# Performance work log

Hardware: AMD Instinct MI355X
Metric: run time of the kernel (lower is better)

The kernel has to match this reference:

```python
import jax, jax.numpy as jnp
import numpy as np

NUM_CLASSES = 2
TOP_K = 1500
CONF_THRESH = 0.01
NMS_THRESH = 0.2
VAR0, VAR1 = 0.1, 0.2  # cfg['variance']


def setup_inputs() -> dict:
    key = jax.random.key(0)
    k1, k2, k3 = jax.random.split(key, 3)
    B, P = 32, 76800
    loc_data = jax.random.normal(k1, (B, P, 4), jnp.float32)
    conf_data = jax.random.uniform(k2, (B * P, NUM_CLASSES), jnp.float32)
    prior_data = jax.random.uniform(k3, (P, 4), jnp.float32)
    return {"loc_data": loc_data, "conf_data": conf_data, "prior_data": prior_data}


def _decode(loc, priors):
    # loc, priors: [P,4]; SSD box decode with variances
    cxcy = priors[:, :2] + loc[:, :2] * VAR0 * priors[:, 2:]
    wh = priors[:, 2:] * jnp.exp(loc[:, 2:] * VAR1)
    x1y1 = cxcy - wh * 0.5
    return jnp.concatenate([x1y1, x1y1 + wh], axis=-1)  # [P,4] (x1,y1,x2,y2)


def _nms_per_class(scores, boxes):
    # scores: [P], boxes: [P,4] -> [TOP_K,5] packed (score,x1,y1,x2,y2)
    s = jnp.where(scores > CONF_THRESH, scores, -jnp.inf)
    sk, idx = jax.lax.top_k(s, TOP_K)  # torch nms keeps only top_k candidates
    bk = boxes[idx]
    x1, y1, x2, y2 = bk[:, 0], bk[:, 1], bk[:, 2], bk[:, 3]
    area = (x2 - x1) * (y2 - y1)
    iota = jnp.arange(TOP_K)

    def step(active, i):
        # greedy NMS over score-descending candidates
        xx1 = jnp.maximum(x1, x1[i]); yy1 = jnp.maximum(y1, y1[i])
        xx2 = jnp.minimum(x2, x2[i]); yy2 = jnp.minimum(y2, y2[i])
        inter = jnp.maximum(xx2 - xx1, 0.0) * jnp.maximum(yy2 - yy1, 0.0)
        iou = inter / (area + area[i] - inter)
        kept = active[i]
        suppress = (iou > NMS_THRESH) & (iota != i)
        active = jnp.where(kept, active & ~suppress, active)
        return active, kept

    _, keep = jax.lax.scan(step, sk > -jnp.inf, iota)
    rows = jnp.where(keep[:, None], jnp.concatenate([sk[:, None], bk], axis=1), 0.0)
    # pack kept rows at the front (score-descending order), zeros after
    rank = jnp.cumsum(keep) - 1
    dest = jnp.where(keep, rank, TOP_K)  # dump non-kept into scratch slot
    return jnp.zeros((TOP_K + 1, 5), bk.dtype).at[dest].set(rows)[:TOP_K]


def reference(loc_data, conf_data, prior_data):
    B, P, _ = loc_data.shape
    conf = conf_data.reshape(B, P, NUM_CLASSES)
    decoded = jax.vmap(_decode, in_axes=(0, None))(loc_data, prior_data)  # [B,P,4]
    outs = []
    for cl in range(1, NUM_CLASSES):  # background class 0 stays zero
        outs.append(jax.vmap(_nms_per_class)(conf[:, :, cl], decoded))
    bg = jnp.zeros((B, 1, TOP_K, 5), decoded.dtype)
    return jnp.concatenate([bg, jnp.stack(outs, axis=1)], axis=1)  # [B,C,TOP_K,5]
```

## Files before the change

### kernel.cpp

```cpp
#include <hip/hip_runtime.h>
#include <stdint.h>

typedef unsigned long long u64;
typedef unsigned int u32;

#define NUM_B 32
#define NUM_P 76800
#define TOPK 1500
#define NBINS 2048
#define CAP 2048
#define NWORDS 24
#define NCHUNK 6
#define HSLICES 16
#define HCHUNK (NUM_P / HSLICES)
#define NPAIR 276

__device__ __forceinline__ u32 fbits(float f) { return __float_as_uint(f); }
__device__ __forceinline__ int binOf(float s) {
    int b = (int)(s * (float)NBINS);
    return (b > NBINS - 1) ? NBINS - 1 : b;
}
__device__ __forceinline__ u64 readlane64(u64 v, int l) {
    u32 lo = (u32)__builtin_amdgcn_readlane((int)(u32)(v & 0xffffffffu), l);
    u32 hi = (u32)__builtin_amdgcn_readlane((int)(u32)(v >> 32), l);
    return ((u64)hi << 32) | lo;
}

__global__ __launch_bounds__(256) void hist_kernel(const float4* __restrict__ conf4,
                                                   u32* __restrict__ hist,
                                                   u32* __restrict__ bpos) {
    int c = blockIdx.x, b = blockIdx.y, tid = threadIdx.x;
    if (tid < NBINS / HSLICES) bpos[(size_t)b * NBINS + c * (NBINS / HSLICES) + tid] = 0;
    __shared__ u32 h[NBINS];
    for (int i = tid; i < NBINS; i += 256) h[i] = 0;
    __syncthreads();
    const float4* base = conf4 + (size_t)b * (NUM_P / 2) + (size_t)c * (HCHUNK / 2);
    for (int i = tid; i < HCHUNK / 2; i += 256) {
        float4 v = base[i];
        if (v.y > 0.01f) atomicAdd(&h[binOf(v.y)], 1u);
        if (v.w > 0.01f) atomicAdd(&h[binOf(v.w)], 1u);
    }
    __syncthreads();
    u32* outp = hist + ((size_t)b * HSLICES + c) * NBINS;
    for (int i = tid; i < NBINS; i += 256) outp[i] = h[i];
}

__global__ void thresh_kernel(const u32* __restrict__ hist, int* __restrict__ tbin,
                              u32* __restrict__ binbase, u32* __restrict__ bincnt,
                              u32* __restrict__ ntotal) {
    int b = blockIdx.x;
    int tid = threadIdx.x;
    const u32* hb = hist + (size_t)b * HSLICES * NBINS;
    __shared__ u32 vals[256];
    __shared__ int s_min;
    u32 total = 0;
    for (int c = 0; c < NBINS / 256; ++c) {
        if (tid == 0) s_min = 256;
        int bin = NBINS - 1 - (c * 256 + tid);
        u32 v = 0;
#pragma unroll
        for (int s = 0; s < HSLICES; ++s) v += hb[(size_t)s * NBINS + bin];
        __syncthreads();
        vals[tid] = v;
        __syncthreads();
        for (int off = 1; off < 256; off <<= 1) {
            u32 add = (tid >= off) ? vals[tid - off] : 0;
            __syncthreads();
            vals[tid] += add;
            __syncthreads();
        }
        u32 cum = total + vals[tid];
        binbase[(size_t)b * NBINS + bin] = cum - v;
        bincnt [(size_t)b * NBINS + bin] = v;
        if (cum >= TOPK) atomicMin(&s_min, tid);
        __syncthreads();
        if (s_min < 256) {
            if (tid == s_min) { tbin[b] = bin; ntotal[b] = cum; }
            return;
        }
        total += vals[255];
    }
    if (tid == 0) { tbin[b] = 0; ntotal[b] = total; }
}

__global__ __launch_bounds__(256) void compact_kernel(
    const float4* __restrict__ conf4, const int* __restrict__ tbin,
    const u32* __restrict__ binbase, u32* __restrict__ bpos,
    u64* __restrict__ keys) {
    int b = blockIdx.y;
    int tid = threadIdx.x;
    int f4 = blockIdx.x * 256 + tid;
    float4 c = conf4[(size_t)b * (NUM_P / 2) + f4];
    int tb = tbin[b];
    int p0 = f4 * 2, p1 = p0 + 1;

    int b0 = binOf(c.y);
    if (c.y > 0.01f && b0 >= tb) {
        u32 slot = atomicAdd(&bpos[(size_t)b * NBINS + b0], 1u);
        u32 pos = binbase[(size_t)b * NBINS + b0] + slot;
        if (pos < CAP) keys[(size_t)b * CAP + pos] = ((u64)fbits(c.y) << 32) | (u32)(~p0);
    }
    int b1 = binOf(c.w);
    if (c.w > 0.01f && b1 >= tb) {
        u32 slot = atomicAdd(&bpos[(size_t)b * NBINS + b1], 1u);
        u32 pos = binbase[(size_t)b * NBINS + b1] + slot;
        if (pos < CAP) keys[(size_t)b * CAP + pos] = ((u64)fbits(c.w) << 32) | (u32)(~p1);
    }
}

__global__ __launch_bounds__(256) void rank_decode_kernel(
    const u64* __restrict__ keys, const u32* __restrict__ binbase,
    const u32* __restrict__ bincnt, const u32* __restrict__ ntotal,
    const float* __restrict__ loc, const float* __restrict__ prior,
    float* __restrict__ sscore, float* __restrict__ sbox) {
#pragma clang fp contract(off)
    int b = blockIdx.y;
    int g = blockIdx.x * 256 + threadIdx.x;
    int n = (int)min(ntotal[b], (u32)CAP);
    if (g >= n) return;
    const u64* kb = keys + (size_t)b * CAP;
    u64 mykey = kb[g];
    float sc = __uint_as_float((u32)(mykey >> 32));
    int bn = binOf(sc);
    u32 start = binbase[(size_t)b * NBINS + bn];
    u32 end = start + bincnt[(size_t)b * NBINS + bn];
    if (end > (u32)n) end = (u32)n;
    u32 rank = start;
#pragma unroll 4
    for (u32 j = start; j < end; ++j) rank += (kb[j] > mykey) ? 1u : 0u;

    if (rank < TOPK) {
        u32 pidx = ~(u32)mykey;
        const float* lp = &loc[((size_t)b * NUM_P + pidx) * 4];
        const float* pp = &prior[(size_t)pidx * 4];
        float lx = lp[0], ly = lp[1], lw = lp[2], lh = lp[3];
        float pcx = pp[0], pcy = pp[1], pw = pp[2], ph = pp[3];
        float cx = pcx + (lx * 0.1f) * pw;
        float cy = pcy + (ly * 0.1f) * ph;
        float w  = pw * expf(lw * 0.2f);
        float h  = ph * expf(lh * 0.2f);
        float x1 = cx - w * 0.5f;
        float y1 = cy - h * 0.5f;
        float x2 = x1 + w;
        float y2 = y1 + h;
        sscore[(size_t)b * TOPK + rank] = sc;
        float* bx = &sbox[((size_t)b * TOPK + rank) * 4];
        bx[0] = x1; bx[1] = y1; bx[2] = x2; bx[3] = y2;
    }
}

__global__ __launch_bounds__(256) void mask_kernel(
    const float* __restrict__ sbox, u64* __restrict__ mask) {
#pragma clang fp contract(off)
    int w = blockIdx.x, c = blockIdx.y, b = blockIdx.z, tid = threadIdx.x;
    int i = c * 256 + tid;
    if ((w * 64 + 63) <= (c * 256)) return;
    __shared__ float4 cbox[64];
    __shared__ float car[64];
    if (tid < 64) {
        int j = w * 64 + tid;
        float4 bx = make_float4(0.f, 0.f, 0.f, 0.f);
        if (j < TOPK) bx = ((const float4*)sbox)[(size_t)b * TOPK + j];
        cbox[tid] = bx;
        car[tid] = (bx.z - bx.x) * (bx.w - bx.y);
    }
    __syncthreads();
    if (i < TOPK && (w * 64 + 63) > i) {
        const double MID = 0.5 * ((double)__uint_as_float(0x3E4CCCCDu) +
                                  (double)__uint_as_float(0x3E4CCCCEu));
        const float4 bx = ((const float4*)sbox)[(size_t)b * TOPK + i];
        float x1i = bx.x, y1i = bx.y, x2i = bx.z, y2i = bx.w;
        float ai = (x2i - x1i) * (y2i - y1i);
        u64 jmask = (i < w * 64) ? ~0ULL : (~0ULL << (i - w * 64 + 1));
        u64 m = 0;
        for (int j2 = 0; j2 < 64; ++j2) {
            float4 cb = cbox[j2];
            float xx1 = fmaxf(cb.x, x1i);
            float yy1 = fmaxf(cb.y, y1i);
            float xx2 = fminf(cb.z, x2i);
            float yy2 = fminf(cb.w, y2i);
            float iw = fmaxf(xx2 - xx1, 0.0f);
            float ih = fmaxf(yy2 - yy1, 0.0f);
            float inter = iw * ih;
            float denom = (car[j2] + ai) - inter;
            if ((double)inter >= MID * (double)denom) m |= (1ULL << j2);
        }
        m &= jmask;
        mask[((size_t)b * NWORDS + w) * TOPK + i] = m;
    }
}

__global__ __launch_bounds__(256) void sweep_kernel(
    const u64* __restrict__ mask, const float* __restrict__ sscore,
    const float* __restrict__ sbox, float* __restrict__ out) {
    int b = blockIdx.x, tid = threadIdx.x;
    int lane = tid & 63, wid = tid >> 6;

    const u64* mbase = mask + (size_t)b * NWORDS * TOPK;

    __shared__ u64 tb[NPAIR * 65];
    __shared__ u64 aw[NWORDS];
    __shared__ u32 pfx[NWORDS + 1];

    u64 act = 0;
    u64 dr[NWORDS];

    if (wid == 0) {
#pragma unroll
        for (int t = 0; t < NWORDS; ++t)
            dr[t] = mbase[(size_t)t * TOPK + t * 64 + lane];
        float sv[NWORDS];
#pragma unroll
        for (int c = 0; c < NWORDS; ++c) {
            int r = c * 64 + lane;
            sv[c] = (r < TOPK) ? sscore[(size_t)b * TOPK + r] : 0.0f;
        }
#pragma unroll
        for (int c = 0; c < NWORDS; ++c) {
            u64 m = __ballot(sv[c] > 0.0f);
            if (lane == c) act = m;
        }
    } else {
        int p0 = (wid - 1) * 92;
        int t = 0, rm = p0;
        while (rm >= NWORDS - 1 - t) { rm -= NWORDS - 1 - t; ++t; }
        int w = t + 1 + rm;
        int pbase = p0;
        for (int ch = 0; ch < 11; ++ch) {
            u64 tmp[8]; int lo[8];
#pragma unroll
            for (int k = 0; k < 8; ++k) {
                tmp[k] = mbase[(size_t)w * TOPK + t * 64 + lane];
                lo[k] = (pbase + k) * 65 + lane;
                if (++w == NWORDS) { ++t; w = t + 1; }
            }
#pragma unroll
            for (int k = 0; k < 8; ++k) tb[lo[k]] = tmp[k];
            pbase += 8;
        }
        {
            u64 tmp[4]; int lo[4];
#pragma unroll
            for (int k = 0; k < 4; ++k) {
                tmp[k] = mbase[(size_t)w * TOPK + t * 64 + lane];
                lo[k] = (pbase + k) * 65 + lane;
                if (++w == NWORDS) { ++t; w = t + 1; }
            }
#pragma unroll
            for (int k = 0; k < 4; ++k) tb[lo[k]] = tmp[k];
        }
    }
    __syncthreads();

    if (wid == 0) {
#pragma unroll
        for (int T = 0; T < NWORDS; ++T) {
            u64 dreg = dr[T];
            u64 actw = readlane64(act, T);
            u64 kept = 0, rem = actw;
            while (rem) {
                int i2 = __ffsll(rem) - 1;
                kept |= (1ULL << i2);
                rem &= rem - 1;
                rem &= ~readlane64(dreg, i2);
            }
            if (lane == T) act = kept;
            if (lane > T && lane < NWORDS) {
                const u64* rb = &tb[((T * (47 - T)) / 2 + (lane - T - 1)) * 65];
                u64 acc = 0;
#pragma unroll
                for (int b16 = 0; b16 < 4; ++b16) {
                    if ((u32)(kept >> (b16 * 16)) & 0xffffu) {
#pragma unroll
                        for (int j = 0; j < 16; ++j) {
                            int r = b16 * 16 + j;
                            u64 sel = (u64)0 - ((kept >> r) & 1ULL);
                            acc |= rb[r] & sel;
                        }
                    }
                }
                act &= ~acc;
            }
        }
        if (lane < NWORDS) aw[lane] = act;
    } else {
        float4* pz = (float4*)(out + (size_t)b * 2 * TOPK * 5);
        float4 z4 = make_float4(0.f, 0.f, 0.f, 0.f);
        for (int t2 = tid - 64; t2 < (2 * TOPK * 5) / 4; t2 += 192) pz[t2] = z4;
    }
    __syncthreads();
    if (tid == 0) {
        u32 acc = 0;
        for (int wd = 0; wd < NWORDS; ++wd) { pfx[wd] = acc; acc += (u32)__popcll(aw[wd]); }
        pfx[NWORDS] = acc;
    }
    __syncthreads();
    for (int r = tid; r < TOPK; r += 256) {
        int wd = r >> 6;
        u64 word = aw[wd];
        if ((word >> (r & 63)) & 1ULL) {
            u32 rank = pfx[wd] + (u32)__popcll(word & ((1ULL << (r & 63)) - 1ULL));
            float sc = sscore[(size_t)b * TOPK + r];
            float4 bx = ((const float4*)sbox)[(size_t)b * TOPK + r];
            size_t base_o = (((size_t)b * 2 + 1) * TOPK + (size_t)rank) * 5;
            out[base_o + 0] = sc;
            out[base_o + 1] = bx.x;
            out[base_o + 2] = bx.y;
            out[base_o + 3] = bx.z;
            out[base_o + 4] = bx.w;
        }
    }
}

extern "C" void kernel_launch(void* const* d_in, const int* in_sizes, int n_in,
                              void* d_out, int out_size, void* d_ws, size_t ws_size,
                              hipStream_t stream) {
    const float* loc   = (const float*)d_in[0];
    const float* conf  = (const float*)d_in[1];
    const float* prior = (const float*)d_in[2];
    float* out = (float*)d_out;
    char* ws = (char*)d_ws;

    u64* mask_buf = (u64*)(ws + 0);
    u32* hist     = (u32*)(ws + 0);
    u32* binbase  = (u32*)(ws + 4194304);
    u32* bincnt   = (u32*)(ws + 4456448);
    u32* bpos     = (u32*)(ws + 4718592);
    u64* keys     = (u64*)(ws + 4980736);
    int* tbin     = (int*)(ws + 5505024);
    u32* ntotal   = (u32*)(ws + 5505152);
    float* sscore = (float*)(ws + 9216000);
    float* sbox   = (float*)(ws + 9408000);

    hist_kernel<<<dim3(HSLICES, 32), 256, 0, stream>>>((const float4*)conf, hist, bpos);
    thresh_kernel<<<32, 256, 0, stream>>>(hist, tbin, binbase, bincnt, ntotal);
    compact_kernel<<<dim3(150, 32), 256, 0, stream>>>((const float4*)conf, tbin, binbase,
                                                      bpos, keys);
    rank_decode_kernel<<<dim3(CAP / 256, 32), 256, 0, stream>>>(keys, binbase, bincnt,
                                                                ntotal, loc, prior,
                                                                sscore, sbox);
    mask_kernel<<<dim3(NWORDS, NCHUNK, 32), 256, 0, stream>>>(sbox, mask_buf);
    sweep_kernel<<<32, 256, 0, stream>>>(mask_buf, sscore, sbox, out);
}
```

Measured before the change: 195.2 us.

## Parallelize NMS sweep diagonal resolution and cross-word suppression across wave lanes

Within the single-wave sequential NMS sweep, each diagonal 64-box block is now pre-resolved with wave-wide OR reductions. Boxes not suppressed by any active box are kept at once, and only the remaining unsafe candidates go through the serial ffs loop. The cross-word suppression OR over 64 rows, previously done by up to 23 lanes each scanning 64 rows, is split across lane groups and combined with shuffle trees. This shortens the serial critical path but adds shuffle and reduction overhead on each of the 24 steps. Lane 63 of the diagonal load is zeroed, apparently to avoid reading beyond valid data.

```diff
diff --git a/kernel.cpp b/kernel.cpp
--- a/kernel.cpp
+++ b/kernel.cpp
@@ -24,6 +24,21 @@
     u32 lo = (u32)__builtin_amdgcn_readlane((int)(u32)(v & 0xffffffffu), l);
     u32 hi = (u32)__builtin_amdgcn_readlane((int)(u32)(v >> 32), l);
     return ((u64)hi << 32) | lo;
+}
+__device__ __forceinline__ u64 shfl64(u64 v, int src) {
+    u32 lo = (u32)__shfl((int)(u32)(v & 0xffffffffu), src, 64);
+    u32 hi = (u32)__shfl((int)(u32)(v >> 32), src, 64);
+    return ((u64)hi << 32) | lo;
+}
+__device__ __forceinline__ u64 shflxor64(u64 v, int m) {
+    u32 lo = (u32)__shfl_xor((int)(u32)(v & 0xffffffffu), m, 64);
+    u32 hi = (u32)__shfl_xor((int)(u32)(v >> 32), m, 64);
+    return ((u64)hi << 32) | lo;
+}
+__device__ __forceinline__ u64 wave_or64(u64 v) {
+#pragma unroll
+    for (int s = 1; s < 64; s <<= 1) v |= shflxor64(v, s);
+    return v;
 }
 
 __global__ __launch_bounds__(256) void hist_kernel(const float4* __restrict__ conf4,
@@ -208,7 +223,7 @@
     if (wid == 0) {
 #pragma unroll
         for (int t = 0; t < NWORDS; ++t)
-            dr[t] = mbase[(size_t)t * TOPK + t * 64 + lane];
+            dr[t] = (lane < 63) ? mbase[(size_t)t * TOPK + t * 64 + lane] : 0ULL;
         float sv[NWORDS];
 #pragma unroll
         for (int c = 0; c < NWORDS; ++c) {
@@ -257,29 +272,47 @@
         for (int T = 0; T < NWORDS; ++T) {
             u64 dreg = dr[T];
             u64 actw = readlane64(act, T);
-            u64 kept = 0, rem = actw;
-            while (rem) {
-                int i2 = __ffsll(rem) - 1;
-                kept |= (1ULL << i2);
-                rem &= rem - 1;
-                rem &= ~readlane64(dreg, i2);
+            u64 mybit = (actw >> lane) & 1ULL;
+            u64 sup = wave_or64(mybit ? dreg : 0ULL);
+            u64 safe = actw & ~sup;
+            u64 unsafe = actw & sup;
+            u64 kept = safe;
+            if (unsafe) {
+                u64 msafe = wave_or64(((safe >> lane) & 1ULL) ? dreg : 0ULL);
+                u64 rem = unsafe & ~msafe;
+                while (rem) {
+                    int i2 = __ffsll(rem) - 1;
+                    kept |= (1ULL << i2);
+                    rem &= rem - 1;
+                    rem &= ~readlane64(dreg, i2);
+                }
             }
             if (lane == T) act = kept;
-            if (lane > T && lane < NWORDS) {
-                const u64* rb = &tb[((T * (47 - T)) / 2 + (lane - T - 1)) * 65];
+            const int nw = NWORDS - 1 - T;
+            if (nw > 0) {
+                const int G = (nw <= 1) ? 64 : (nw <= 2) ? 32 : (nw <= 4) ? 16
+                             : (nw <= 8) ? 8 : (nw <= 16) ? 4 : 2;
+                const int R = 64 / G;
+                int g = lane / nw;
+                int w = lane - g * nw;
                 u64 acc = 0;
-#pragma unroll
-                for (int b16 = 0; b16 < 4; ++b16) {
-                    if ((u32)(kept >> (b16 * 16)) & 0xffffu) {
-#pragma unroll
-                        for (int j = 0; j < 16; ++j) {
-                            int r = b16 * 16 + j;
-                            u64 sel = (u64)0 - ((kept >> r) & 1ULL);
-                            acc |= rb[r] & sel;
-                        }
+                if (g < G) {
+                    const u64* rbB = &tb[(size_t)(((T * (47 - T)) / 2 + w) * 65)];
+                    int r0 = g * R;
+#pragma unroll
+                    for (int jj = 0; jj < R; ++jj) {
+                        int r = r0 + jj;
+                        u64 sel = (u64)0 - ((kept >> r) & 1ULL);
+                        acc |= rbB[r] & sel;
                     }
                 }
-                act &= ~acc;
+#pragma unroll
+                for (int s = 1; s < G; s <<= 1)
+                    acc |= shfl64(acc, (g ^ s) * nw + w);
+                int srcl = lane - T - 1;
+                srcl = (srcl < 0 || srcl >= nw) ? 0 : srcl;
+                u64 supw = shfl64(acc, srcl);
+                if (lane > T && lane < NWORDS) act &= ~supw;
             }
         }
         if (lane < NWORDS) aw[lane] = act;
```

New measurement: 194.2 us. Within noise of the previous version (-0.6%).

## Widen sweep kernel to 1024 threads and add sparse-kept mask OR path

Applied to the files above, without the earlier changes.

The sweep kernel now launches 1024 threads per batch, so 15 loader waves each stage 19 mask tiles into shared memory instead of 3 waves staging 92, and the output zeroing moves into the load phase. Diagonal mask words are staged in shared memory rather than held in 24 registers, and the outer word loop is no longer unrolled, to relieve register pressure. The cross-word suppression uses a bit-iteration path when few boxes are kept, which avoids the full 64-row OR. Only 32 blocks are launched, so the serial wave-0 sweep remains the critical path, and the extra shared-memory reads may add latency.

```diff
diff --git a/kernel.cpp b/kernel.cpp
--- a/kernel.cpp
+++ b/kernel.cpp
@@ -190,7 +190,7 @@
     }
 }
 
-__global__ __launch_bounds__(256) void sweep_kernel(
+__global__ __launch_bounds__(1024) void sweep_kernel(
     const u64* __restrict__ mask, const float* __restrict__ sscore,
     const float* __restrict__ sbox, float* __restrict__ out) {
     int b = blockIdx.x, tid = threadIdx.x;
@@ -199,16 +199,18 @@
     const u64* mbase = mask + (size_t)b * NWORDS * TOPK;
 
     __shared__ u64 tb[NPAIR * 65];
+    __shared__ u64 td[NWORDS * 65];
     __shared__ u64 aw[NWORDS];
     __shared__ u32 pfx[NWORDS + 1];
 
     u64 act = 0;
-    u64 dr[NWORDS];
 
     if (wid == 0) {
 #pragma unroll
-        for (int t = 0; t < NWORDS; ++t)
-            dr[t] = mbase[(size_t)t * TOPK + t * 64 + lane];
+        for (int t = 0; t < NWORDS; ++t) {
+            u64 v = (lane < 63) ? mbase[(size_t)t * TOPK + t * 64 + lane] : 0ULL;
+            td[t * 65 + lane] = v;
+        }
         float sv[NWORDS];
 #pragma unroll
         for (int c = 0; c < NWORDS; ++c) {
@@ -221,41 +223,35 @@
             if (lane == c) act = m;
         }
     } else {
-        int p0 = (wid - 1) * 92;
+        int cnt = (wid == 15) ? (NPAIR - 14 * 19) : 19;
+        int p0 = (wid - 1) * 19;
         int t = 0, rm = p0;
         while (rm >= NWORDS - 1 - t) { rm -= NWORDS - 1 - t; ++t; }
         int w = t + 1 + rm;
-        int pbase = p0;
-        for (int ch = 0; ch < 11; ++ch) {
+        for (int base = 0; base < cnt; base += 8) {
+            int m = cnt - base; if (m > 8) m = 8;
             u64 tmp[8]; int lo[8];
 #pragma unroll
             for (int k = 0; k < 8; ++k) {
-                tmp[k] = mbase[(size_t)w * TOPK + t * 64 + lane];
-                lo[k] = (pbase + k) * 65 + lane;
-                if (++w == NWORDS) { ++t; w = t + 1; }
+                if (k < m) {
+                    tmp[k] = mbase[(size_t)w * TOPK + t * 64 + lane];
+                    lo[k] = (p0 + base + k) * 65 + lane;
+                    if (++w == NWORDS) { ++t; w = t + 1; }
+                }
             }
 #pragma unroll
-            for (int k = 0; k < 8; ++k) tb[lo[k]] = tmp[k];
-            pbase += 8;
-        }
-        {
-            u64 tmp[4]; int lo[4];
-#pragma unroll
-            for (int k = 0; k < 4; ++k) {
-                tmp[k] = mbase[(size_t)w * TOPK + t * 64 + lane];
-                lo[k] = (pbase + k) * 65 + lane;
-                if (++w == NWORDS) { ++t; w = t + 1; }
-            }
-#pragma unroll
-            for (int k = 0; k < 4; ++k) tb[lo[k]] = tmp[k];
-        }
+            for (int k = 0; k < 8; ++k) if (k < m) tb[lo[k]] = tmp[k];
+        }
+        float4* pz = (float4*)(out + (size_t)b * 2 * TOPK * 5);
+        float4 z4 = make_float4(0.f, 0.f, 0.f, 0.f);
+        for (int t2 = tid - 64; t2 < (2 * TOPK * 5) / 4; t2 += 960) pz[t2] = z4;
     }
     __syncthreads();
 
     if (wid == 0) {
-#pragma unroll
+#pragma unroll 1
         for (int T = 0; T < NWORDS; ++T) {
-            u64 dreg = dr[T];
+            u64 dreg = td[T * 65 + lane];
             u64 actw = readlane64(act, T);
             u64 kept = 0, rem = actw;
             while (rem) {
@@ -266,27 +262,26 @@
             }
             if (lane == T) act = kept;
             if (lane > T && lane < NWORDS) {
-                const u64* rb = &tb[((T * (47 - T)) / 2 + (lane - T - 1)) * 65];
-                u64 acc = 0;
-#pragma unroll
-                for (int b16 = 0; b16 < 4; ++b16) {
-                    if ((u32)(kept >> (b16 * 16)) & 0xffffu) {
-#pragma unroll
-                        for (int j = 0; j < 16; ++j) {
-                            int r = b16 * 16 + j;
-                            u64 sel = (u64)0 - ((kept >> r) & 1ULL);
-                            acc |= rb[r] & sel;
-                        }
+                const u64* rb = &tb[(size_t)((T * (47 - T)) / 2 + (lane - T - 1)) * 65];
+                if (__popcll(kept) > 4) {
+                    u64 acc = 0;
+#pragma unroll 16
+                    for (int j = 0; j < 64; ++j) {
+                        u64 sel = (u64)0 - ((kept >> j) & 1ULL);
+                        acc |= rb[j] & sel;
+                    }
+                    act &= ~acc;
+                } else {
+                    u64 kb = kept;
+                    while (kb) {
+                        int r = __ffsll(kb) - 1;
+                        kb &= kb - 1;
+                        act &= ~rb[r];
                     }
                 }
-                act &= ~acc;
             }
         }
         if (lane < NWORDS) aw[lane] = act;
-    } else {
-        float4* pz = (float4*)(out + (size_t)b * 2 * TOPK * 5);
-        float4 z4 = make_float4(0.f, 0.f, 0.f, 0.f);
-        for (int t2 = tid - 64; t2 < (2 * TOPK * 5) / 4; t2 += 192) pz[t2] = z4;
     }
     __syncthreads();
     if (tid == 0) {
@@ -295,7 +290,7 @@
         pfx[NWORDS] = acc;
     }
     __syncthreads();
-    for (int r = tid; r < TOPK; r += 256) {
+    for (int r = tid; r < TOPK; r += 1024) {
         int wd = r >> 6;
         u64 word = aw[wd];
         if ((word >> (r & 63)) & 1ULL) {
@@ -340,5 +335,5 @@
                                                                 ntotal, loc, prior,
                                                                 sscore, sbox);
     mask_kernel<<<dim3(NWORDS, NCHUNK, 32), 256, 0, stream>>>(sbox, mask_buf);
-    sweep_kernel<<<32, 256, 0, stream>>>(mask_buf, sscore, sbox, out);
-}
+    sweep_kernel<<<32, 1024, 0, stream>>>(mask_buf, sscore, sbox, out);
+}
```

After: 194.9 us. No clear change (-0.2%).
